# Kernel tuning notes

Hardware: AMD Instinct MI355X
Metric: run time of the kernel (lower is better)

## Reference

```python
import jax, jax.numpy as jnp
import numpy as np

HIDDEN = 4096
N_HEADS = 32
N_KV_HEADS = 8
HEAD_DIM = 128
ROPE_THETA = 10000.0


def setup_inputs() -> dict:
    key = jax.random.key(0)
    ks = jax.random.split(key, 5)
    B, S = 1, 2048
    scale = 0.02
    return {
        "hidden_states": jax.random.normal(ks[0], (B, S, HIDDEN), dtype=jnp.float32),
        "q_w": jax.random.normal(ks[1], (N_HEADS * HEAD_DIM, HIDDEN), dtype=jnp.float32) * scale,
        "k_w": jax.random.normal(ks[2], (N_KV_HEADS * HEAD_DIM, HIDDEN), dtype=jnp.float32) * scale,
        "v_w": jax.random.normal(ks[3], (N_KV_HEADS * HEAD_DIM, HIDDEN), dtype=jnp.float32) * scale,
        "o_w": jax.random.normal(ks[4], (HIDDEN, N_HEADS * HEAD_DIM), dtype=jnp.float32) * scale,
        "position_ids": jnp.arange(S, dtype=jnp.int64 if jax.config.jax_enable_x64 else jnp.int32)[None, :],
    }


def _rotate_half(x):
    h = x.shape[-1] // 2
    return jnp.concatenate((-x[..., h:], x[..., :h]), axis=-1)


def _rope_cos_sin(position_ids, dtype):
    # default rope: inv_freq = theta^(-arange(0,hd,2)/hd), attention_scaling = 1
    inv_freq = 1.0 / (ROPE_THETA ** (jnp.arange(0, HEAD_DIM, 2, dtype=jnp.float32) / HEAD_DIM))
    freqs = position_ids.astype(jnp.float32)[:, :, None] * inv_freq[None, None, :]  # [B,S,hd/2]
    emb = jnp.concatenate((freqs, freqs), axis=-1)  # [B,S,hd]
    return jnp.cos(emb).astype(dtype), jnp.sin(emb).astype(dtype)


def reference(hidden_states, q_w, k_w, v_w, o_w, position_ids):
    B, S, _ = hidden_states.shape
    n_rep = N_HEADS // N_KV_HEADS

    q = (hidden_states @ q_w.T).reshape(B, S, N_HEADS, HEAD_DIM).transpose(0, 2, 1, 3)
    k = (hidden_states @ k_w.T).reshape(B, S, N_KV_HEADS, HEAD_DIM).transpose(0, 2, 1, 3)
    v = (hidden_states @ v_w.T).reshape(B, S, N_KV_HEADS, HEAD_DIM).transpose(0, 2, 1, 3)

    cos, sin = _rope_cos_sin(position_ids, hidden_states.dtype)
    cos = cos[:, None, :, :]  # unsqueeze head dim
    sin = sin[:, None, :, :]
    q = q * cos + _rotate_half(q) * sin
    k = k * cos + _rotate_half(k) * sin

    # repeat_kv (GQA)
    k = jnp.repeat(k, n_rep, axis=1)  # [B,H,S,hd]
    v = jnp.repeat(v, n_rep, axis=1)

    scale = HEAD_DIM ** -0.5
    scores = jnp.einsum("bhqd,bhkd->bhqk", q, k) * scale  # [B,H,S,S]
    causal = jnp.tril(jnp.ones((S, S), dtype=bool))
    scores = jnp.where(causal[None, None, :, :], scores, jnp.finfo(scores.dtype).min)
    probs = jax.nn.softmax(scores, axis=-1)
    attn = jnp.einsum("bhqk,bhkd->bhqd", probs, v)  # [B,H,S,hd]

    attn = attn.transpose(0, 2, 1, 3).reshape(B, S, N_HEADS * HEAD_DIM)
    return attn @ o_w.T
```

## Files before the change

kernel.cpp:

```cpp
#include <hip/hip_runtime.h>
#include <hip/hip_bf16.h>

#define NH   32
#define NKV  8
#define HD   128
#define SL   2048
#define HID  4096
#define KVW  1024
#define QKVN 6144

typedef __attribute__((ext_vector_type(8))) short short8;
typedef __attribute__((ext_vector_type(4))) float f32x4;

static __device__ __forceinline__ unsigned short f2bf(float f){
  union { float f; unsigned int i; } v; v.f = f;
  unsigned int r = v.i + 0x7FFFu + ((v.i >> 16) & 1u);
  return (unsigned short)(r >> 16);
}
static __device__ __forceinline__ float bf2f(unsigned short u){
  union { unsigned int i; float f; } v; v.i = ((unsigned int)u) << 16; return v.f;
}
static __device__ __forceinline__ unsigned int pack2(float lo, float hi){
  return (unsigned int)f2bf(lo) | ((unsigned int)f2bf(hi) << 16);
}
static __device__ __forceinline__ unsigned int cvtpk(float lo, float hi){
  unsigned int d;
  asm("v_cvt_pk_bf16_f32 %0, %1, %2" : "=v"(d) : "v"(lo), "v"(hi));
  return d;
}

static __device__ __forceinline__ void gload_lds16(const void* g, void* l){
  __builtin_amdgcn_global_load_lds(
      (const __attribute__((address_space(1))) void*)g,
      (__attribute__((address_space(3))) void*)l,
      16, 0, 0);
}

__global__ void cast_f32_bf16(const float* __restrict__ src, uint4* __restrict__ dst, int n8){
  int stride = gridDim.x * blockDim.x;
  for (int i = blockIdx.x * blockDim.x + threadIdx.x; i < n8; i += stride){
    float4 a = ((const float4*)src)[2*i + 0];
    float4 b = ((const float4*)src)[2*i + 1];
    uint4 o;
    o.x = pack2(a.x, a.y); o.y = pack2(a.z, a.w);
    o.z = pack2(b.x, b.y); o.w = pack2(b.z, b.w);
    dst[i] = o;
  }
}

__global__ void rope_table_kernel(const int* __restrict__ pos, float2* __restrict__ tab){
  int i = blockIdx.x * blockDim.x + threadIdx.x;
  if (i >= SL * 64) return;
  int s = i >> 6, f = i & 63;
  float inv = expf(-((float)(2 * f) / 128.0f) * 9.210340371976184f);
  float ang = (float)pos[s] * inv;
  float sn, cs;
  sincosf(ang, &sn, &cs);
  tab[i] = make_float2(cs, sn);
}

__global__ void rope_apply_kernel(unsigned short* x, const float2* __restrict__ tab,
                                  int nheads, int rowstride){
  int i = blockIdx.x * blockDim.x + threadIdx.x;
  int total = SL * nheads * 64;
  if (i >= total) return;
  int f = i & 63;
  int t = i >> 6;
  int h = t % nheads;
  int s = t / nheads;
  float2 cs = tab[s * 64 + f];
  size_t base = (size_t)s * rowstride + h * HD;
  float x1 = bf2f(x[base + f]);
  float x2 = bf2f(x[base + f + 64]);
  x[base + f]      = f2bf(x1 * cs.x - x2 * cs.y);
  x[base + f + 64] = f2bf(x2 * cs.x + x1 * cs.y);
}

template<int BN, bool F32OUT>
__global__ __launch_bounds__(256) void gemm_bt(
  const unsigned short* __restrict__ A,
  const unsigned short* __restrict__ B,
  void* __restrict__ Cp, int M, int N, int K)
{
  constexpr int NFR = BN / 32;
  __shared__ __align__(16) unsigned short As[2][128 * 32];
  __shared__ __align__(16) unsigned short Bs[2][BN * 32];
  const int tid = threadIdx.x;
  const int lane = tid & 63, wid = tid >> 6;
  const int g = lane >> 4, c15 = lane & 15;
  const int wr = wid >> 1, wc = wid & 1;

  const int gx = gridDim.x, gy = gridDim.y;
  const int nwg = gx * gy;
  const int lin = blockIdx.y * gx + blockIdx.x;
  int mb, nb;
  const int cpx = nwg >> 3;
  const int RN  = cpx >> 3;
  if (RN > 0 && (gy & 7) == 0 && (cpx & 7) == 0 && gx % RN == 0 && (8 % (gx / RN)) == 0){
    int xcd = lin & 7, j = lin >> 3;
    int nrc = gx / RN;
    int rr = xcd / nrc, rc = xcd % nrc;
    mb = rr * 8 + (j & 7);
    nb = rc * RN + (j >> 3);
  } else { mb = lin / gx; nb = lin % gx; }
  const int m0 = mb * 128, n0 = nb * BN;

  const int srowA = wid * 32 + (lane >> 2);
  const int srowB = wid * (BN / 4) + (lane >> 2);
  const int scol  = (lane & 3) * 8;
  const unsigned short* Ag = &A[(size_t)(m0 + srowA) * K + scol];
  const unsigned short* Bg = &B[(size_t)(n0 + srowB) * K + scol];
  const size_t K16 = (size_t)16 * K;

  f32x4 acc[4][NFR] = {};

  gload_lds16(Ag,       &As[0][wid * 1024]);
  gload_lds16(Ag + K16, &As[0][wid * 1024 + 512]);
#pragma unroll
  for (int q = 0; q < BN / 64; ++q)
    gload_lds16(Bg + q * K16, &Bs[0][wid * (BN / 4) * 32 + q * 512]);
  __syncthreads();

  const int nk = K >> 5;
  for (int t = 0; t < nk; ++t){
    const int cur = t & 1;
    if (t + 1 < nk){
      const unsigned short* a2 = Ag + (size_t)(t + 1) * 32;
      const unsigned short* b2 = Bg + (size_t)(t + 1) * 32;
      const int nb2 = cur ^ 1;
      gload_lds16(a2,       &As[nb2][wid * 1024]);
      gload_lds16(a2 + K16, &As[nb2][wid * 1024 + 512]);
#pragma unroll
      for (int q = 0; q < BN / 64; ++q)
        gload_lds16(b2 + q * K16, &Bs[nb2][wid * (BN / 4) * 32 + q * 512]);
    }
    short8 af[4], bfr[NFR];
#pragma unroll
    for (int m = 0; m < 4; ++m)
      af[m] = *(const short8*)(&As[cur][(wr * 64 + m * 16 + c15) * 32 + g * 8]);
#pragma unroll
    for (int n = 0; n < NFR; ++n)
      bfr[n] = *(const short8*)(&Bs[cur][(wc * (BN / 2) + n * 16 + c15) * 32 + g * 8]);
#pragma unroll
    for (int m = 0; m < 4; ++m)
#pragma unroll
      for (int n = 0; n < NFR; ++n)
        acc[m][n] = __builtin_amdgcn_mfma_f32_16x16x32_bf16(af[m], bfr[n], acc[m][n], 0, 0, 0);
    __syncthreads();
  }

#pragma unroll
  for (int m = 0; m < 4; ++m)
#pragma unroll
    for (int n = 0; n < NFR; ++n){
      int row = m0 + wr * 64 + m * 16 + g * 4;
      int col = n0 + wc * (BN / 2) + n * 16 + c15;
      f32x4 v = acc[m][n];
      if (F32OUT){
        float* C = (float*)Cp;
#pragma unroll
        for (int r = 0; r < 4; ++r) C[(size_t)(row + r) * N + col] = v[r];
      } else {
        unsigned short* C = (unsigned short*)Cp;
#pragma unroll
        for (int r = 0; r < 4; ++r) C[(size_t)(row + r) * N + col] = f2bf(v[r]);
      }
    }
}

__global__ void transpose_v_kernel(const unsigned short* __restrict__ v, int vstride,
                                   unsigned short* __restrict__ vt){
  __shared__ unsigned short t[64][65];
  int h  = blockIdx.z;
  int d0 = blockIdx.y * 64;
  int s0 = blockIdx.x * 64;
  int c  = threadIdx.x & 63;
  int r0 = threadIdx.x >> 6;
#pragma unroll
  for (int r = r0; r < 64; r += 4) t[r][c] = v[(size_t)(s0 + r) * vstride + h * HD + d0 + c];
  __syncthreads();
#pragma unroll
  for (int r = r0; r < 64; r += 4) vt[(size_t)(h * HD + d0 + r) * SL + s0 + c] = t[c][r];
}

__global__ __launch_bounds__(512, 4) void flash_attn_kernel(
  const unsigned short* __restrict__ Q,
  const unsigned short* __restrict__ Kb,
  const unsigned short* __restrict__ Vt,
  unsigned short* __restrict__ O)
{
  __shared__ __align__(16) unsigned short Ks[64 * 128];
  __shared__ __align__(16) unsigned short Vs[128 * 64];
  const int tid = threadIdx.x, lane = tid & 63, wid = tid >> 6;
  const int g = lane >> 4, c15 = lane & 15;
  const int kvh = blockIdx.x;
  const int yy = blockIdx.y;
  const int qb = (yy < 32) ? (63 - yy) : (yy - 32);
  const int h = kvh * 4 + (wid & 3);
  const int rg = wid >> 2;
  const int q0 = qb * 32;
  const int qg = q0 + rg * 16 + c15;

  short8 aq[4];
  {
    size_t qrow = (size_t)qg * QKVN + h * HD;
#pragma unroll
    for (int kk = 0; kk < 4; ++kk)
      aq[kk] = *(const short8*)(&Q[qrow + kk * 32 + g * 8]);
  }

  const int krow = tid >> 3, kcol = (tid & 7) * 8;
  const int vrow = tid >> 2, vcol = (tid & 3) * 8;
  const unsigned short* Kgb = Kb + (size_t)kvh * HD;
  const unsigned short* Vgb = Vt + ((size_t)kvh * HD + vrow) * SL;

  uint4 kr0, kr1, vr0, vr1;
  {
    const unsigned short* kg = Kgb + (size_t)krow * QKVN + kcol;
    kr0 = *(const uint4*)kg; kr1 = *(const uint4*)(kg + 64);
    const unsigned short* vg = Vgb + vcol;
    vr0 = *(const uint4*)vg; vr1 = *(const uint4*)(vg + 32);
  }

  float m_i = -1e30f, l_i = 0.f;
  f32x4 oacc[8];
#pragma unroll
  for (int df = 0; df < 8; ++df) oacc[df] = (f32x4){0.f, 0.f, 0.f, 0.f};

  const float scl2 = 0.08838834764831845f * 1.4426950408889634f;
  const int nt = (q0 + 31) / 64 + 1;
  for (int kt = 0; kt < nt; ++kt){
    *(uint4*)((char*)Ks + krow * 256 + (( kcol * 2       ) ^ ((krow & 7) << 4))) = kr0;
    *(uint4*)((char*)Ks + krow * 256 + (((kcol * 2) + 128) ^ ((krow & 7) << 4))) = kr1;
    *(uint4*)((char*)Vs + vrow * 128 + (( vcol * 2       ) ^ ((vrow & 7) << 4))) = vr0;
    *(uint4*)((char*)Vs + vrow * 128 + (((vcol * 2) +  64) ^ ((vrow & 7) << 4))) = vr1;
    __syncthreads();

    if (kt + 1 < nt){
      const unsigned short* kg = Kgb + (size_t)((kt + 1) * 64 + krow) * QKVN + kcol;
      kr0 = *(const uint4*)kg; kr1 = *(const uint4*)(kg + 64);
      const unsigned short* vg = Vgb + (kt + 1) * 64 + vcol;
      vr0 = *(const uint4*)vg; vr1 = *(const uint4*)(vg + 32);
    }

    f32x4 sc[4];
    __builtin_amdgcn_s_setprio(1);
#pragma unroll
    for (int f = 0; f < 4; ++f){
      sc[f] = (f32x4){0.f, 0.f, 0.f, 0.f};
#pragma unroll
      for (int kk = 0; kk < 4; ++kk){
        short8 bk = *(const short8*)((const char*)Ks + (f * 16 + c15) * 256 +
                                     ((kk * 64 + g * 16) ^ ((c15 & 7) << 4)));
        sc[f] = __builtin_amdgcn_mfma_f32_16x16x32_bf16(bk, aq[kk], sc[f], 0, 0, 0);
      }
    }
    __builtin_amdgcn_s_setprio(0);

    float p[4][4];
#pragma unroll
    for (int f = 0; f < 4; ++f)
#pragma unroll
      for (int r = 0; r < 4; ++r){
        int kvg = kt * 64 + f * 16 + g * 4 + r;
        p[f][r] = (kvg <= qg) ? sc[f][r] * scl2 : -1e30f;
      }

    float pmax = p[0][0];
#pragma unroll
    for (int f = 0; f < 4; ++f)
#pragma unroll
      for (int r = 0; r < 4; ++r) pmax = fmaxf(pmax, p[f][r]);
    pmax = fmaxf(pmax, __shfl_xor(pmax, 16, 64));
    pmax = fmaxf(pmax, __shfl_xor(pmax, 32, 64));

    if (!__all(pmax - m_i <= 8.0f)){
      float mnew = fmaxf(m_i, pmax);
      float cf = exp2f(m_i - mnew);
      float cfr[4];
#pragma unroll
      for (int r = 0; r < 4; ++r) cfr[r] = __shfl(cf, (lane & 48) | (g * 4 + r), 64);
#pragma unroll
      for (int df = 0; df < 8; ++df)
#pragma unroll
        for (int r = 0; r < 4; ++r) oacc[df][r] *= cfr[r];
      l_i *= cf;
      m_i = mnew;
    }

    float lsum = 0.f;
#pragma unroll
    for (int f = 0; f < 4; ++f)
#pragma unroll
      for (int r = 0; r < 4; ++r){ float e = exp2f(p[f][r] - m_i); p[f][r] = e; lsum += e; }
    lsum += __shfl_xor(lsum, 16, 64);
    lsum += __shfl_xor(lsum, 32, 64);
    l_i += lsum;

    unsigned int pd[4][2];
#pragma unroll
    for (int f = 0; f < 4; ++f){
      pd[f][0] = cvtpk(p[f][0], p[f][1]);
      pd[f][1] = cvtpk(p[f][2], p[f][3]);
    }

    const int src0 = ((g & 1) << 5) | c15;
    const int src1 = src0 + 16;
    const bool hiF = (g >= 2);
#pragma unroll
    for (int kk = 0; kk < 2; ++kk){
      union { unsigned int u[4]; short8 s8; } pa;
#pragma unroll
      for (int pr = 0; pr < 2; ++pr){
        unsigned int a0 = __shfl((int)pd[2 * kk + 0][pr], src0, 64);
        unsigned int b0 = __shfl((int)pd[2 * kk + 1][pr], src0, 64);
        unsigned int a1 = __shfl((int)pd[2 * kk + 0][pr], src1, 64);
        unsigned int b1 = __shfl((int)pd[2 * kk + 1][pr], src1, 64);
        pa.u[pr]     = hiF ? b0 : a0;
        pa.u[2 + pr] = hiF ? b1 : a1;
      }
      __builtin_amdgcn_s_setprio(1);
#pragma unroll
      for (int df = 0; df < 8; ++df){
        short8 bv = *(const short8*)((const char*)Vs + (df * 16 + c15) * 128 +
                                     ((kk * 64 + g * 16) ^ ((c15 & 7) << 4)));
        oacc[df] = __builtin_amdgcn_mfma_f32_16x16x32_bf16(pa.s8, bv, oacc[df], 0, 0, 0);
      }
      __builtin_amdgcn_s_setprio(0);
    }
    __syncthreads();
  }

  float lr[4];
#pragma unroll
  for (int r = 0; r < 4; ++r) lr[r] = __shfl(l_i, (lane & 48) | (g * 4 + r), 64);
#pragma unroll
  for (int df = 0; df < 8; ++df)
#pragma unroll
    for (int r = 0; r < 4; ++r){
      int row = q0 + rg * 16 + g * 4 + r;
      O[(size_t)row * HID + h * HD + df * 16 + c15] = f2bf(oacc[df][r] / lr[r]);
    }
}

extern "C" void kernel_launch(void* const* d_in, const int* in_sizes, int n_in,
                              void* d_out, int out_size, void* d_ws, size_t ws_size,
                              hipStream_t stream)
{
  const float* hs  = (const float*)d_in[0];
  const float* qw  = (const float*)d_in[1];
  const float* kw  = (const float*)d_in[2];
  const float* vw  = (const float*)d_in[3];
  const float* ow  = (const float*)d_in[4];
  const int*   pos = (const int*)d_in[5];

  char* w = (char*)d_ws;
  auto alloc = [&](size_t bytes){ char* p = w; w += (bytes + 255) & ~(size_t)255; return p; };
  unsigned short* xb   = (unsigned short*)alloc((size_t)SL * HID * 2);
  unsigned short* wqkv = (unsigned short*)alloc((size_t)QKVN * HID * 2);
  unsigned short* owb  = (unsigned short*)alloc((size_t)HID * HID * 2);
  unsigned short* qkv  = (unsigned short*)alloc((size_t)SL * QKVN * 2);
  unsigned short* vt   = (unsigned short*)alloc((size_t)SL * KVW * 2);
  unsigned short* ab   = (unsigned short*)alloc((size_t)SL * HID * 2);
  float2*         tab  = (float2*)alloc((size_t)SL * 64 * sizeof(float2));

  auto cast = [&](const float* s, unsigned short* d, long n){
    int n8 = (int)(n / 8);
    int blocks = (n8 + 255) / 256; if (blocks > 2048) blocks = 2048;
    cast_f32_bf16<<<blocks, 256, 0, stream>>>(s, (uint4*)d, n8);
  };
  cast(hs, xb, (long)SL * HID);
  cast(qw, wqkv,                              (long)HID * HID);
  cast(kw, wqkv + (size_t)HID * HID,          (long)KVW * HID);
  cast(vw, wqkv + (size_t)(HID + KVW) * HID,  (long)KVW * HID);
  cast(ow, owb,                               (long)HID * HID);

  rope_table_kernel<<<(SL * 64 + 255) / 256, 256, 0, stream>>>(pos, tab);

  gemm_bt<128, false><<<dim3(QKVN / 128, SL / 128), 256, 0, stream>>>(xb, wqkv, qkv, SL, QKVN, HID);

  rope_apply_kernel<<<(SL * 40 * 64 + 255) / 256, 256, 0, stream>>>(qkv, tab, 40, QKVN);

  transpose_v_kernel<<<dim3(SL / 64, HD / 64, NKV), 256, 0, stream>>>(qkv + HID + KVW, QKVN, vt);

  flash_attn_kernel<<<dim3(NKV, SL / 32), 512, 0, stream>>>(qkv, qkv + HID, vt, ab);

  gemm_bt<128, true><<<dim3(HID / 128, SL / 128), 256, 0, stream>>>(ab, owb, d_out, SL, HID, HID);
}
```

Baseline: 347.8 us.

## Double-buffer K/V in LDS, skip causal mask on full tiles, vectorize RoPE

The flash attention kernel now keeps two LDS buffers for K and V, so the next tile is written while the current one is consumed. This removes one barrier per iteration and hides LDS store latency, with global loads prefetched two tiles ahead. Tiles that lie entirely below the causal diagonal skip the per-element mask compare. The RoPE apply kernel is vectorized to 8 elements per thread using 16-byte loads and stores. The cost is doubled LDS use per block (32KB), which may lower occupancy under launch_bounds(512,4).

```diff
diff --git a/kernel.cpp b/kernel.cpp
--- a/kernel.cpp
+++ b/kernel.cpp
@@ -62,18 +62,27 @@
 __global__ void rope_apply_kernel(unsigned short* x, const float2* __restrict__ tab,
                                   int nheads, int rowstride){
   int i = blockIdx.x * blockDim.x + threadIdx.x;
-  int total = SL * nheads * 64;
+  int total = SL * nheads * 8;
   if (i >= total) return;
-  int f = i & 63;
-  int t = i >> 6;
+  int fb = (i & 7) * 8;
+  int t = i >> 3;
   int h = t % nheads;
   int s = t / nheads;
-  float2 cs = tab[s * 64 + f];
   size_t base = (size_t)s * rowstride + h * HD;
-  float x1 = bf2f(x[base + f]);
-  float x2 = bf2f(x[base + f + 64]);
-  x[base + f]      = f2bf(x1 * cs.x - x2 * cs.y);
-  x[base + f + 64] = f2bf(x2 * cs.x + x1 * cs.y);
+  short8 x1 = *(const short8*)&x[base + fb];
+  short8 x2 = *(const short8*)&x[base + fb + 64];
+  const float2* tb = &tab[s * 64 + fb];
+  short8 o1, o2;
+#pragma unroll
+  for (int j = 0; j < 8; ++j){
+    float2 cs = tb[j];
+    float a = bf2f((unsigned short)x1[j]);
+    float b = bf2f((unsigned short)x2[j]);
+    o1[j] = (short)f2bf(a * cs.x - b * cs.y);
+    o2[j] = (short)f2bf(b * cs.x + a * cs.y);
+  }
+  *(short8*)&x[base + fb]      = o1;
+  *(short8*)&x[base + fb + 64] = o2;
 }
 
 template<int BN, bool F32OUT>
@@ -189,8 +198,8 @@
   const unsigned short* __restrict__ Vt,
   unsigned short* __restrict__ O)
 {
-  __shared__ __align__(16) unsigned short Ks[64 * 128];
-  __shared__ __align__(16) unsigned short Vs[128 * 64];
+  __shared__ __align__(16) unsigned short Ks[2][64 * 128];
+  __shared__ __align__(16) unsigned short Vs[2][128 * 64];
   const int tid = threadIdx.x, lane = tid & 63, wid = tid >> 6;
   const int g = lane >> 4, c15 = lane & 15;
   const int kvh = blockIdx.x;
@@ -214,13 +223,18 @@
   const unsigned short* Kgb = Kb + (size_t)kvh * HD;
   const unsigned short* Vgb = Vt + ((size_t)kvh * HD + vrow) * SL;
 
-  uint4 kr0, kr1, vr0, vr1;
-  {
-    const unsigned short* kg = Kgb + (size_t)krow * QKVN + kcol;
-    kr0 = *(const uint4*)kg; kr1 = *(const uint4*)(kg + 64);
-    const unsigned short* vg = Vgb + vcol;
-    vr0 = *(const uint4*)vg; vr1 = *(const uint4*)(vg + 32);
-  }
+  auto loadKV = [&](int kt, uint4& a, uint4& b, uint4& c, uint4& d){
+    const unsigned short* kg = Kgb + (size_t)(kt * 64 + krow) * QKVN + kcol;
+    a = *(const uint4*)kg; b = *(const uint4*)(kg + 64);
+    const unsigned short* vg = Vgb + kt * 64 + vcol;
+    c = *(const uint4*)vg; d = *(const uint4*)(vg + 32);
+  };
+  auto writeKV = [&](int buf, uint4 a, uint4 b, uint4 c, uint4 d){
+    *(uint4*)((char*)&Ks[buf][0] + krow * 256 + (( kcol * 2       ) ^ ((krow & 7) << 4))) = a;
+    *(uint4*)((char*)&Ks[buf][0] + krow * 256 + (((kcol * 2) + 128) ^ ((krow & 7) << 4))) = b;
+    *(uint4*)((char*)&Vs[buf][0] + vrow * 128 + (( vcol * 2       ) ^ ((vrow & 7) << 4))) = c;
+    *(uint4*)((char*)&Vs[buf][0] + vrow * 128 + (((vcol * 2) +  64) ^ ((vrow & 7) << 4))) = d;
+  };
 
   float m_i = -1e30f, l_i = 0.f;
   f32x4 oacc[8];
@@ -229,19 +243,17 @@
 
   const float scl2 = 0.08838834764831845f * 1.4426950408889634f;
   const int nt = (q0 + 31) / 64 + 1;
+
+  uint4 kr0, kr1, vr0, vr1;
+  loadKV(0, kr0, kr1, vr0, vr1);
+  writeKV(0, kr0, kr1, vr0, vr1);
+  if (nt > 1) loadKV(1, kr0, kr1, vr0, vr1);
+  __syncthreads();
+
   for (int kt = 0; kt < nt; ++kt){
-    *(uint4*)((char*)Ks + krow * 256 + (( kcol * 2       ) ^ ((krow & 7) << 4))) = kr0;
-    *(uint4*)((char*)Ks + krow * 256 + (((kcol * 2) + 128) ^ ((krow & 7) << 4))) = kr1;
-    *(uint4*)((char*)Vs + vrow * 128 + (( vcol * 2       ) ^ ((vrow & 7) << 4))) = vr0;
-    *(uint4*)((char*)Vs + vrow * 128 + (((vcol * 2) +  64) ^ ((vrow & 7) << 4))) = vr1;
-    __syncthreads();
-
-    if (kt + 1 < nt){
-      const unsigned short* kg = Kgb + (size_t)((kt + 1) * 64 + krow) * QKVN + kcol;
-      kr0 = *(const uint4*)kg; kr1 = *(const uint4*)(kg + 64);
-      const unsigned short* vg = Vgb + (kt + 1) * 64 + vcol;
-      vr0 = *(const uint4*)vg; vr1 = *(const uint4*)(vg + 32);
-    }
+    const int cur = kt & 1, nxt = cur ^ 1;
+    if (kt + 1 < nt) writeKV(nxt, kr0, kr1, vr0, vr1);
+    if (kt + 2 < nt) loadKV(kt + 2, kr0, kr1, vr0, vr1);
 
     f32x4 sc[4];
     __builtin_amdgcn_s_setprio(1);
@@ -250,7 +262,7 @@
       sc[f] = (f32x4){0.f, 0.f, 0.f, 0.f};
 #pragma unroll
       for (int kk = 0; kk < 4; ++kk){
-        short8 bk = *(const short8*)((const char*)Ks + (f * 16 + c15) * 256 +
+        short8 bk = *(const short8*)((const char*)&Ks[cur][0] + (f * 16 + c15) * 256 +
                                      ((kk * 64 + g * 16) ^ ((c15 & 7) << 4)));
         sc[f] = __builtin_amdgcn_mfma_f32_16x16x32_bf16(bk, aq[kk], sc[f], 0, 0, 0);
       }
@@ -258,13 +270,20 @@
     __builtin_amdgcn_s_setprio(0);
 
     float p[4][4];
-#pragma unroll
-    for (int f = 0; f < 4; ++f)
-#pragma unroll
-      for (int r = 0; r < 4; ++r){
-        int kvg = kt * 64 + f * 16 + g * 4 + r;
-        p[f][r] = (kvg <= qg) ? sc[f][r] * scl2 : -1e30f;
-      }
+    if (kt * 64 + 63 <= q0 + rg * 16){
+#pragma unroll
+      for (int f = 0; f < 4; ++f)
+#pragma unroll
+        for (int r = 0; r < 4; ++r) p[f][r] = sc[f][r] * scl2;
+    } else {
+#pragma unroll
+      for (int f = 0; f < 4; ++f)
+#pragma unroll
+        for (int r = 0; r < 4; ++r){
+          int kvg = kt * 64 + f * 16 + g * 4 + r;
+          p[f][r] = (kvg <= qg) ? sc[f][r] * scl2 : -1e30f;
+        }
+    }
 
     float pmax = p[0][0];
 #pragma unroll
@@ -322,7 +341,7 @@
       __builtin_amdgcn_s_setprio(1);
 #pragma unroll
       for (int df = 0; df < 8; ++df){
-        short8 bv = *(const short8*)((const char*)Vs + (df * 16 + c15) * 128 +
+        short8 bv = *(const short8*)((const char*)&Vs[cur][0] + (df * 16 + c15) * 128 +
                                      ((kk * 64 + g * 16) ^ ((c15 & 7) << 4)));
         oacc[df] = __builtin_amdgcn_mfma_f32_16x16x32_bf16(pa.s8, bv, oacc[df], 0, 0, 0);
       }
@@ -379,7 +398,7 @@
 
   gemm_bt<128, false><<<dim3(QKVN / 128, SL / 128), 256, 0, stream>>>(xb, wqkv, qkv, SL, QKVN, HID);
 
-  rope_apply_kernel<<<(SL * 40 * 64 + 255) / 256, 256, 0, stream>>>(qkv, tab, 40, QKVN);
+  rope_apply_kernel<<<(SL * 40 * 8 + 255) / 256, 256, 0, stream>>>(qkv, tab, 40, QKVN);
 
   transpose_v_kernel<<<dim3(SL / 64, HD / 64, NKV), 256, 0, stream>>>(qkv + HID + KVW, QKVN, vt);
 
```

Result: no change. 343.9 us (-1.1%).
